# Optimization experiments

Measured on AMD Instinct MI355X. Metric: run time of the kernel, lower is better.

The kernel has to match this reference:

```python
import jax, jax.numpy as jnp
import numpy as np

B, S, D, H, E, K = 4, 1024, 1024, 4096, 8, 2

def setup_inputs() -> dict:
    key = jax.random.key(0)
    ks = jax.random.split(key, 6)
    sd = 1.0 / np.sqrt(D)
    sh = 1.0 / np.sqrt(H)
    return {
        "x": jax.random.normal(ks[0], (B, S, D), jnp.float32),
        "Wg": jax.random.normal(ks[1], (D, E), jnp.float32) * sd,
        "bg": jnp.zeros((E,), jnp.float32),
        "W1": jax.random.normal(ks[2], (E, D, H), jnp.float32) * sd,
        "b1": jnp.zeros((E, H), jnp.float32),
        "Wa": jax.random.normal(ks[3], (E, D, H), jnp.float32) * sd,
        "ba": jnp.zeros((E, H), jnp.float32),
        "W2": jax.random.normal(ks[4], (E, H, D), jnp.float32) * sh,
        "b2": jnp.zeros((E, D), jnp.float32),
        "kv_cache": 0,
    }

def reference(x, Wg, bg, W1, b1, Wa, ba, W2, b2, kv_cache):
    # gate: softmax over experts, top-k, renormalize
    gate = jax.nn.softmax(x @ Wg + bg, axis=-1)            # [B,S,E]
    w, idx = jax.lax.top_k(gate, K)                        # [B,S,K]
    w = w / jnp.sum(w, axis=-1, keepdims=True)
    # dense all-expert FF with SwiGLU: fc2( silu(fc_a(x)) * fc1(x) )
    a = jnp.einsum('bsd,edh->bseh', x, Wa) + ba            # [B,S,E,H]
    g = a * jax.nn.sigmoid(a)
    u = jnp.einsum('bsd,edh->bseh', x, W1) + b1
    y = jnp.einsum('bseh,ehd->bsed', g * u, W2) + b2       # [B,S,E,D]
    # gather top-k experts per token and combine
    sel = jnp.take_along_axis(y, idx[..., None], axis=2)   # [B,S,K,D]
    out = jnp.sum(sel * w[..., None], axis=-2)             # [B,S,D]
    return out
```

## Files before the change

### kernel.cpp

```cpp
#include <hip/hip_runtime.h>
#include <hip/hip_bf16.h>
#include <math.h>

#define TOKENS 4096
#define DD 1024
#define HH 4096
#define NE 8
#define PAIRS 8192
#define ROWCAP 8448
#define TCAP 72
#define G1_NT 32
#define G2_NT 128

typedef __bf16 bf16x8 __attribute__((ext_vector_type(8)));
typedef float f32x4 __attribute__((ext_vector_type(4)));

__device__ __forceinline__ unsigned short f2bf(float f) {
  union { float f; unsigned int u; } c; c.f = f;
  unsigned int x = c.u;
  return (unsigned short)((x + 0x7fffu + ((x >> 16) & 1u)) >> 16);
}

__device__ __forceinline__ void lds16(void* l, const void* g) {
  __builtin_amdgcn_global_load_lds((const __attribute__((address_space(1))) void*)g,
                                   (__attribute__((address_space(3))) void*)l, 16, 0, 0);
}

__global__ void init_kernel(int* counts) {
  if (threadIdx.x < NE) counts[threadIdx.x] = 0;
}

__global__ __launch_bounds__(256) void transpose_kernel(
    const float* __restrict__ Wa, const float* __restrict__ W1, const float* __restrict__ W2,
    unsigned short* __restrict__ WaT, unsigned short* __restrict__ W1T,
    unsigned short* __restrict__ W2T) {
  int b = blockIdx.x;
  int sec = b >> 13;
  int sb = b & 8191;
  const float* in; unsigned short* out; int R, C;
  if (sec == 0)      { in = Wa; out = WaT; R = DD; C = HH; }
  else if (sec == 1) { in = W1; out = W1T; R = DD; C = HH; }
  else               { in = W2; out = W2T; R = HH; C = DD; }
  int ntr = R >> 6, ntc = C >> 6;
  int per_e = ntr * ntc;
  int e = sb / per_e;
  int rem = sb - e * per_e;
  int tr = rem / ntc, tc = rem - (rem / ntc) * ntc;
  const float* ie = in + (size_t)e * R * C;
  unsigned short* oe = out + (size_t)e * R * C;

  __shared__ float t[64][68];
  int tid = threadIdx.x;
  int lr = tid >> 2;
  int c4 = (tid & 3) << 4;
  const float* src = ie + (size_t)(tr * 64 + lr) * C + tc * 64 + c4;
  float4 v0 = *(const float4*)(src);
  float4 v1 = *(const float4*)(src + 4);
  float4 v2 = *(const float4*)(src + 8);
  float4 v3 = *(const float4*)(src + 12);
  *(float4*)&t[lr][c4] = v0;
  *(float4*)&t[lr][c4 + 4] = v1;
  *(float4*)&t[lr][c4 + 8] = v2;
  *(float4*)&t[lr][c4 + 12] = v3;
  __syncthreads();

  int oc = tid >> 2;
  int r0 = (tid & 3) << 4;
  unsigned int pk[8];
#pragma unroll
  for (int i = 0; i < 8; i++) {
    unsigned int lo = f2bf(t[r0 + 2 * i][oc]);
    unsigned int hi = f2bf(t[r0 + 2 * i + 1][oc]);
    pk[i] = lo | (hi << 16);
  }
  unsigned short* dst = oe + (size_t)(tc * 64 + oc) * R + tr * 64 + r0;
  *(uint4*)(dst) = make_uint4(pk[0], pk[1], pk[2], pk[3]);
  *(uint4*)(dst + 8) = make_uint4(pk[4], pk[5], pk[6], pk[7]);
}

__global__ __launch_bounds__(256) void gate_kernel(const float* __restrict__ x,
    const float* __restrict__ Wg, const float* __restrict__ bg,
    int* __restrict__ counts, int* __restrict__ tok_e, int* __restrict__ tok_slot,
    float* __restrict__ tok_w) {
  int t = blockIdx.x, tid = threadIdx.x;
  const float* xr = x + (size_t)t * DD;
  float p[8] = {0, 0, 0, 0, 0, 0, 0, 0};
  for (int d = tid; d < DD; d += 256) {
    float xv = xr[d];
    const float4* wrow = (const float4*)(Wg + (size_t)d * NE);
    float4 w0 = wrow[0], w1 = wrow[1];
    p[0] += xv * w0.x; p[1] += xv * w0.y; p[2] += xv * w0.z; p[3] += xv * w0.w;
    p[4] += xv * w1.x; p[5] += xv * w1.y; p[6] += xv * w1.z; p[7] += xv * w1.w;
  }
#pragma unroll
  for (int e = 0; e < 8; e++) {
    p[e] += __shfl_down(p[e], 32);
    p[e] += __shfl_down(p[e], 16);
    p[e] += __shfl_down(p[e], 8);
    p[e] += __shfl_down(p[e], 4);
    p[e] += __shfl_down(p[e], 2);
    p[e] += __shfl_down(p[e], 1);
  }
  __shared__ float red[4][8];
  if ((tid & 63) == 0) {
#pragma unroll
    for (int e = 0; e < 8; e++) red[tid >> 6][e] = p[e];
  }
  __syncthreads();
  if (tid == 0) {
    float l[8];
#pragma unroll
    for (int e = 0; e < 8; e++) l[e] = red[0][e] + red[1][e] + red[2][e] + red[3][e] + bg[e];
    int e0 = 0; float l0 = l[0];
    for (int e = 1; e < 8; e++) if (l[e] > l0) { e0 = e; l0 = l[e]; }
    int e1 = -1; float l1 = -3.4e38f;
    for (int e = 0; e < 8; e++) if (e != e0 && l[e] > l1) { e1 = e; l1 = l[e]; }
    float w0 = 1.f / (1.f + __expf(l1 - l0));
    float w1 = 1.f - w0;
    int s0 = atomicAdd(&counts[e0], 1);
    int s1 = atomicAdd(&counts[e1], 1);
    tok_e[2 * t] = e0;     tok_slot[2 * t] = s0;     tok_w[2 * t] = w0;
    tok_e[2 * t + 1] = e1; tok_slot[2 * t + 1] = s1; tok_w[2 * t + 1] = w1;
  }
}

__global__ void scan_kernel(const int* __restrict__ counts, int* __restrict__ offsets,
                            int* __restrict__ tm_e, int* __restrict__ tm_row0,
                            int* __restrict__ tm_nrow, int* __restrict__ ntp) {
  if (threadIdx.x != 0 || blockIdx.x != 0) return;
  int c[NE];
#pragma unroll
  for (int e = 0; e < NE; e++) c[e] = counts[e];
  int off = 0, nt = 0;
  for (int e = 0; e < NE; e++) {
    offsets[e] = off;
    for (int r = 0; r < c[e]; r += 128) {
      tm_e[nt] = e; tm_row0[nt] = off + r;
      tm_nrow[nt] = (c[e] - r < 128) ? (c[e] - r) : 128;
      nt++;
    }
    off += c[e];
  }
  *ntp = nt;
}

__global__ __launch_bounds__(64) void gather_kernel(const float* __restrict__ x,
    const int* __restrict__ tok_e, const int* __restrict__ tok_slot,
    const float* __restrict__ tok_w, const int* __restrict__ offsets,
    unsigned short* __restrict__ Xe, int* __restrict__ pair_row, float* __restrict__ rw) {
  int pp = blockIdx.x, tid = threadIdx.x;
  int e = tok_e[pp];
  int row = offsets[e] + tok_slot[pp];
  int t = pp >> 1;
  const float* src = x + (size_t)t * DD + tid * 16;
  float4 v0 = *(const float4*)(src);
  float4 v1 = *(const float4*)(src + 4);
  float4 v2 = *(const float4*)(src + 8);
  float4 v3 = *(const float4*)(src + 12);
  unsigned int pk[8];
  pk[0] = f2bf(v0.x) | ((unsigned int)f2bf(v0.y) << 16);
  pk[1] = f2bf(v0.z) | ((unsigned int)f2bf(v0.w) << 16);
  pk[2] = f2bf(v1.x) | ((unsigned int)f2bf(v1.y) << 16);
  pk[3] = f2bf(v1.z) | ((unsigned int)f2bf(v1.w) << 16);
  pk[4] = f2bf(v2.x) | ((unsigned int)f2bf(v2.y) << 16);
  pk[5] = f2bf(v2.z) | ((unsigned int)f2bf(v2.w) << 16);
  pk[6] = f2bf(v3.x) | ((unsigned int)f2bf(v3.y) << 16);
  pk[7] = f2bf(v3.z) | ((unsigned int)f2bf(v3.w) << 16);
  unsigned short* dst = Xe + (size_t)row * DD + tid * 16;
  *(uint4*)(dst) = make_uint4(pk[0], pk[1], pk[2], pk[3]);
  *(uint4*)(dst + 8) = make_uint4(pk[4], pk[5], pk[6], pk[7]);
  if (tid == 0) { pair_row[pp] = row; rw[row] = tok_w[pp]; }
}


__global__ __launch_bounds__(256) void gemm1_kernel(
    const unsigned short* __restrict__ Xe,
    const unsigned short* __restrict__ WaT,
    const unsigned short* __restrict__ W1T,
    const float* __restrict__ ba, const float* __restrict__ b1,
    unsigned short* __restrict__ h,
    const int* __restrict__ tm_e, const int* __restrict__ tm_row0,
    const int* __restrict__ tm_nrow, const int* __restrict__ ntp) {
  __shared__ unsigned short sm[2][8192];

  int work = blockIdx.x;
  int tile = work >> 6;
  if (tile >= *ntp) return;
  int n0 = (work & 63) << 6;
  int e = tm_e[tile], row0 = tm_row0[tile], nrow = tm_nrow[tile];

  int tid = threadIdx.x;
  int lane = tid & 63, wid = tid >> 6;
  int wm = wid >> 1, wn = wid & 1;
  int fr = lane & 15, kc = lane >> 4;

  int srow = tid >> 2;
  int cd = tid & 3;
  int scl = (cd ^ ((srow >> 1) & 3)) << 3;

  const unsigned short* pA0 = Xe + (size_t)(row0 + srow) * DD + scl;
  const unsigned short* pA1 = Xe + (size_t)(row0 + 64 + srow) * DD + scl;
  const unsigned short* pBa = WaT + ((size_t)e << 22) + (size_t)(n0 + srow) * DD + scl;
  const unsigned short* pBu = W1T + ((size_t)e << 22) + (size_t)(n0 + srow) * DD + scl;

  unsigned short* ldst = &sm[0][0] + (size_t)tid * 8;

  int aof[4], bof[2];
#pragma unroll
  for (int m = 0; m < 4; m++) {
    int r = wm * 64 + m * 16 + fr;
    aof[m] = r * 64 + ((kc ^ ((r >> 1) & 3)) << 4);
  }
#pragma unroll
  for (int n = 0; n < 2; n++) {
    int r = wn * 32 + n * 16 + fr;
    bof[n] = 8192 + r * 64 + ((kc ^ ((r >> 1) & 3)) << 4);
  }

  f32x4 accA[4][2], accU[4][2];
  f32x4 z = {0.f, 0.f, 0.f, 0.f};
#pragma unroll
  for (int m = 0; m < 4; m++)
#pragma unroll
    for (int n = 0; n < 2; n++) { accA[m][n] = z; accU[m][n] = z; }

  auto stage = [&](int T, int buf) {
    int koff = (T < G1_NT ? T : G1_NT - 1) << 5;
    unsigned short* L = ldst + buf * 8192;
    lds16(L, pA0 + koff);
    lds16(L + 2048, pA1 + koff);
    lds16(L + 4096, pBa + koff);
    lds16(L + 6144, pBu + koff);
  };

  stage(0, 0);
  __syncthreads();
  int buf = 0;
  for (int T = 0; T < G1_NT; ++T) {
    stage(T + 1, buf ^ 1);
    const char* lb = (const char*)&sm[0][0] + (buf << 14);
    bf16x8 a[4], bA[2], bU[2];
#pragma unroll
    for (int m = 0; m < 4; m++) a[m] = *(const bf16x8*)(lb + aof[m]);
#pragma unroll
    for (int n = 0; n < 2; n++) {
      bA[n] = *(const bf16x8*)(lb + bof[n]);
      bU[n] = *(const bf16x8*)(lb + bof[n] + 4096);
    }
#pragma unroll
    for (int m = 0; m < 4; m++)
#pragma unroll
      for (int n = 0; n < 2; n++) {
        accA[m][n] = __builtin_amdgcn_mfma_f32_16x16x32_bf16(a[m], bA[n], accA[m][n], 0, 0, 0);
        accU[m][n] = __builtin_amdgcn_mfma_f32_16x16x32_bf16(a[m], bU[n], accU[m][n], 0, 0, 0);
      }
    __syncthreads();
    buf ^= 1;
  }

  int lr4 = kc * 4;
#pragma unroll
  for (int n = 0; n < 2; n++) {
    int col = n0 + wn * 32 + n * 16 + fr;
    float bav = ba[e * HH + col];
    float buv = b1[e * HH + col];
#pragma unroll
    for (int m = 0; m < 4; m++) {
#pragma unroll
      for (int j = 0; j < 4; j++) {
        int r = wm * 64 + m * 16 + lr4 + j;
        if (r < nrow) {
          float av = accA[m][n][j] + bav;
          float uv = accU[m][n][j] + buv;
          float s = __builtin_amdgcn_rcpf(1.f + __expf(-av));
          h[(size_t)(row0 + r) * HH + col] = f2bf(av * s * uv);
        }
      }
    }
  }
}

__global__ __launch_bounds__(256) void gemm2_kernel(
    const unsigned short* __restrict__ hb,
    const unsigned short* __restrict__ W2T,
    const float* __restrict__ b2, const float* __restrict__ rw,
    float* __restrict__ contrib,
    const int* __restrict__ tm_e, const int* __restrict__ tm_row0,
    const int* __restrict__ tm_nrow, const int* __restrict__ ntp) {
  __shared__ unsigned short sm[2][8192];

  int work = blockIdx.x;
  int tile = work >> 3;
  if (tile >= *ntp) return;
  int n0 = (work & 7) << 7;
  int e = tm_e[tile], row0 = tm_row0[tile], nrow = tm_nrow[tile];

  int tid = threadIdx.x;
  int lane = tid & 63, wid = tid >> 6;
  int wm = wid >> 1, wn = wid & 1;
  int fr = lane & 15, kc = lane >> 4;

  int srow = tid >> 2;
  int cd = tid & 3;
  int scl = (cd ^ ((srow >> 1) & 3)) << 3;

  const unsigned short* pA0 = hb + (size_t)(row0 + srow) * HH + scl;
  const unsigned short* pA1 = hb + (size_t)(row0 + 64 + srow) * HH + scl;
  const unsigned short* pB0 = W2T + ((size_t)e << 22) + (size_t)(n0 + srow) * HH + scl;
  const unsigned short* pB1 = W2T + ((size_t)e << 22) + (size_t)(n0 + 64 + srow) * HH + scl;

  unsigned short* ldst = &sm[0][0] + (size_t)tid * 8;

  int aof[4], bof[4];
#pragma unroll
  for (int m = 0; m < 4; m++) {
    int r = wm * 64 + m * 16 + fr;
    aof[m] = r * 64 + ((kc ^ ((r >> 1) & 3)) << 4);
  }
#pragma unroll
  for (int n = 0; n < 4; n++) {
    int r = wn * 64 + n * 16 + fr;
    bof[n] = 8192 + r * 64 + ((kc ^ ((r >> 1) & 3)) << 4);
  }

  f32x4 acc[4][4];
  f32x4 z = {0.f, 0.f, 0.f, 0.f};
#pragma unroll
  for (int m = 0; m < 4; m++)
#pragma unroll
    for (int n = 0; n < 4; n++) acc[m][n] = z;

  auto stage = [&](int T, int buf) {
    int koff = (T < G2_NT ? T : G2_NT - 1) << 5;
    unsigned short* L = ldst + buf * 8192;
    lds16(L, pA0 + koff);
    lds16(L + 2048, pA1 + koff);
    lds16(L + 4096, pB0 + koff);
    lds16(L + 6144, pB1 + koff);
  };

  stage(0, 0);
  __syncthreads();
  int buf = 0;
  for (int T = 0; T < G2_NT; ++T) {
    stage(T + 1, buf ^ 1);
    const char* lb = (const char*)&sm[0][0] + (buf << 14);
    bf16x8 a[4], b[4];
#pragma unroll
    for (int m = 0; m < 4; m++) a[m] = *(const bf16x8*)(lb + aof[m]);
#pragma unroll
    for (int n = 0; n < 4; n++) b[n] = *(const bf16x8*)(lb + bof[n]);
#pragma unroll
    for (int m = 0; m < 4; m++)
#pragma unroll
      for (int n = 0; n < 4; n++)
        acc[m][n] = __builtin_amdgcn_mfma_f32_16x16x32_bf16(a[m], b[n], acc[m][n], 0, 0, 0);
    __syncthreads();
    buf ^= 1;
  }

  float b2v[4];
#pragma unroll
  for (int n = 0; n < 4; n++) b2v[n] = b2[e * DD + n0 + wn * 64 + n * 16 + fr];
  int lr4 = kc * 4;
#pragma unroll
  for (int m = 0; m < 4; m++) {
#pragma unroll
    for (int j = 0; j < 4; j++) {
      int r = wm * 64 + m * 16 + lr4 + j;
      if (r < nrow) {
        float wv = rw[row0 + r];
        float* dst = contrib + (size_t)(row0 + r) * DD + n0 + wn * 64 + fr;
#pragma unroll
        for (int n = 0; n < 4; n++)
          dst[n * 16] = wv * (acc[m][n][j] + b2v[n]);
      }
    }
  }
}

__global__ __launch_bounds__(256) void combine_kernel(const float* __restrict__ contrib,
    const int* __restrict__ pair_row, float* __restrict__ out) {
  int t = blockIdx.x, tid = threadIdx.x;
  int r0 = pair_row[2 * t], r1 = pair_row[2 * t + 1];
  const float4* c0 = (const float4*)(contrib + (size_t)r0 * DD);
  const float4* c1 = (const float4*)(contrib + (size_t)r1 * DD);
  float4* o = (float4*)(out + (size_t)t * DD);
  float4 a = c0[tid], b = c1[tid];
  o[tid] = make_float4(a.x + b.x, a.y + b.y, a.z + b.z, a.w + b.w);
}

extern "C" void kernel_launch(void* const* d_in, const int* in_sizes, int n_in,
                              void* d_out, int out_size, void* d_ws, size_t ws_size,
                              hipStream_t stream) {
  const float* x  = (const float*)d_in[0];
  const float* Wg = (const float*)d_in[1];
  const float* bg = (const float*)d_in[2];
  const float* W1 = (const float*)d_in[3];
  const float* b1 = (const float*)d_in[4];
  const float* Wa = (const float*)d_in[5];
  const float* ba = (const float*)d_in[6];
  const float* W2 = (const float*)d_in[7];
  const float* b2 = (const float*)d_in[8];
  float* out = (float*)d_out;
  (void)in_sizes; (void)n_in; (void)out_size; (void)ws_size;

  char* p = (char*)d_ws;
  auto take = [&](size_t bytes) { char* r = p; p += (bytes + 255) & ~(size_t)255; return r; };
  unsigned short* WaT = (unsigned short*)take((size_t)NE * HH * DD * 2);
  unsigned short* W1T = (unsigned short*)take((size_t)NE * HH * DD * 2);
  unsigned short* W2T = (unsigned short*)take((size_t)NE * DD * HH * 2);
  unsigned short* Xe  = (unsigned short*)take((size_t)ROWCAP * DD * 2);
  unsigned short* hb  = (unsigned short*)take((size_t)ROWCAP * HH * 2);
  float* contrib      = (float*)take((size_t)ROWCAP * DD * 4);
  int* counts   = (int*)take(64);
  int* offsets  = (int*)take(64);
  int* tok_e    = (int*)take(PAIRS * 4);
  int* tok_slot = (int*)take(PAIRS * 4);
  float* tok_w  = (float*)take(PAIRS * 4);
  int* pair_row = (int*)take(PAIRS * 4);
  float* rw     = (float*)take(ROWCAP * 4);
  int* tm_e     = (int*)take(TCAP * 4);
  int* tm_row0  = (int*)take(TCAP * 4);
  int* tm_nrow  = (int*)take(TCAP * 4);
  int* ntp      = (int*)take(64);

  init_kernel<<<1, 64, 0, stream>>>(counts);
  transpose_kernel<<<3 * 8192, 256, 0, stream>>>(Wa, W1, W2, WaT, W1T, W2T);
  gate_kernel<<<TOKENS, 256, 0, stream>>>(x, Wg, bg, counts, tok_e, tok_slot, tok_w);
  scan_kernel<<<1, 64, 0, stream>>>(counts, offsets, tm_e, tm_row0, tm_nrow, ntp);
  gather_kernel<<<PAIRS, 64, 0, stream>>>(x, tok_e, tok_slot, tok_w, offsets, Xe, pair_row, rw);
  gemm1_kernel<<<TCAP * 64, 256, 0, stream>>>(Xe, WaT, W1T, ba, b1, hb, tm_e, tm_row0, tm_nrow, ntp);
  gemm2_kernel<<<TCAP * 8, 256, 0, stream>>>(hb, W2T, b2, rw, contrib, tm_e, tm_row0, tm_nrow, ntp);
  combine_kernel<<<TOKENS, 256, 0, stream>>>(contrib, pair_row, out);
}
```

Measured before the change: 556.8 us.

## Enlarge MoE GEMM tiles to 512-thread blocks with 256-row/256-col tiles

Both expert GEMMs move to 512-thread blocks with eight waves. GEMM1 now covers 256 token rows per tile, which needs a separate 256-row tile map from the scan kernel. GEMM2 now covers 256 output columns per tile. The aim is to reuse each staged weight and activation tile across more MFMA work, which cuts global/L2 traffic per FLOP. In exchange, LDS use per block grows to 48KB, there are fewer blocks to spread across CUs, and partially filled 256-row tiles waste more work.

```diff
diff --git a/kernel.cpp b/kernel.cpp
--- a/kernel.cpp
+++ b/kernel.cpp
@@ -8,6 +8,7 @@
 #define NE 8
 #define PAIRS 8192
 #define ROWCAP 8448
+#define T1CAP 40
 #define TCAP 72
 #define G1_NT 32
 #define G2_NT 128
@@ -125,23 +126,31 @@
 }
 
 __global__ void scan_kernel(const int* __restrict__ counts, int* __restrict__ offsets,
-                            int* __restrict__ tm_e, int* __restrict__ tm_row0,
-                            int* __restrict__ tm_nrow, int* __restrict__ ntp) {
+                            int* __restrict__ tm1_e, int* __restrict__ tm1_row0,
+                            int* __restrict__ tm1_nrow, int* __restrict__ ntp1,
+                            int* __restrict__ tm2_e, int* __restrict__ tm2_row0,
+                            int* __restrict__ tm2_nrow, int* __restrict__ ntp2) {
   if (threadIdx.x != 0 || blockIdx.x != 0) return;
   int c[NE];
 #pragma unroll
   for (int e = 0; e < NE; e++) c[e] = counts[e];
-  int off = 0, nt = 0;
+  int off = 0, n1 = 0, n2 = 0;
   for (int e = 0; e < NE; e++) {
     offsets[e] = off;
+    for (int r = 0; r < c[e]; r += 256) {
+      tm1_e[n1] = e; tm1_row0[n1] = off + r;
+      tm1_nrow[n1] = (c[e] - r < 256) ? (c[e] - r) : 256;
+      n1++;
+    }
     for (int r = 0; r < c[e]; r += 128) {
-      tm_e[nt] = e; tm_row0[nt] = off + r;
-      tm_nrow[nt] = (c[e] - r < 128) ? (c[e] - r) : 128;
-      nt++;
+      tm2_e[n2] = e; tm2_row0[n2] = off + r;
+      tm2_nrow[n2] = (c[e] - r < 128) ? (c[e] - r) : 128;
+      n2++;
     }
     off += c[e];
   }
-  *ntp = nt;
+  *ntp1 = n1;
+  *ntp2 = n2;
 }
 
 __global__ __launch_bounds__(64) void gather_kernel(const float* __restrict__ x,
@@ -173,7 +182,7 @@
 }
 
 
-__global__ __launch_bounds__(256) void gemm1_kernel(
+__global__ __launch_bounds__(512, 2) void gemm1_kernel(
     const unsigned short* __restrict__ Xe,
     const unsigned short* __restrict__ WaT,
     const unsigned short* __restrict__ W1T,
@@ -181,7 +190,7 @@
     unsigned short* __restrict__ h,
     const int* __restrict__ tm_e, const int* __restrict__ tm_row0,
     const int* __restrict__ tm_nrow, const int* __restrict__ ntp) {
-  __shared__ unsigned short sm[2][8192];
+  __shared__ unsigned short sm[2][12288];
 
   int work = blockIdx.x;
   int tile = work >> 6;
@@ -190,20 +199,24 @@
   int e = tm_e[tile], row0 = tm_row0[tile], nrow = tm_nrow[tile];
 
   int tid = threadIdx.x;
-  int lane = tid & 63, wid = tid >> 6;
-  int wm = wid >> 1, wn = wid & 1;
-  int fr = lane & 15, kc = lane >> 4;
-
-  int srow = tid >> 2;
-  int cd = tid & 3;
-  int scl = (cd ^ ((srow >> 1) & 3)) << 3;
-
-  const unsigned short* pA0 = Xe + (size_t)(row0 + srow) * DD + scl;
-  const unsigned short* pA1 = Xe + (size_t)(row0 + 64 + srow) * DD + scl;
-  const unsigned short* pBa = WaT + ((size_t)e << 22) + (size_t)(n0 + srow) * DD + scl;
-  const unsigned short* pBu = W1T + ((size_t)e << 22) + (size_t)(n0 + srow) * DD + scl;
-
-  unsigned short* ldst = &sm[0][0] + (size_t)tid * 8;
+  int l = tid & 63, w = tid >> 6;
+  int wm = w >> 1, wn = w & 1;
+  int fr = l & 15, kc = l >> 4;
+
+  int arow = (w << 4) + (l >> 2);
+  int cd = l & 3;
+  int swzA = (cd ^ ((arow >> 1) & 3)) << 3;
+  const unsigned short* pA1 = Xe + (size_t)(row0 + arow) * DD + swzA;
+  const unsigned short* pA2 = pA1 + (size_t)128 * DD;
+  int brow = (w < 4) ? arow : (arow - 64);
+  int swzB = (cd ^ ((brow >> 1) & 3)) << 3;
+  const unsigned short* pB = ((w < 4) ? WaT : W1T) + ((size_t)e << 22) +
+                             (size_t)(n0 + brow) * DD + swzB;
+
+  unsigned short* smb = &sm[0][0];
+  int dA1 = (w << 10) + (l << 4);
+  int dA2 = dA1 + 8192;
+  int dB  = 16384 + ((w & 3) << 10) + ((w >= 4) ? 4096 : 0) + (l << 4);
 
   int aof[4], bof[2];
 #pragma unroll
@@ -214,7 +227,7 @@
 #pragma unroll
   for (int n = 0; n < 2; n++) {
     int r = wn * 32 + n * 16 + fr;
-    bof[n] = 8192 + r * 64 + ((kc ^ ((r >> 1) & 3)) << 4);
+    bof[n] = 16384 + r * 64 + ((kc ^ ((r >> 1) & 3)) << 4);
   }
 
   f32x4 accA[4][2], accU[4][2];
@@ -226,11 +239,10 @@
 
   auto stage = [&](int T, int buf) {
     int koff = (T < G1_NT ? T : G1_NT - 1) << 5;
-    unsigned short* L = ldst + buf * 8192;
-    lds16(L, pA0 + koff);
-    lds16(L + 2048, pA1 + koff);
-    lds16(L + 4096, pBa + koff);
-    lds16(L + 6144, pBu + koff);
+    char* base = (char*)smb + buf * 24576;
+    lds16(base + dA1, pA1 + koff);
+    lds16(base + dA2, pA2 + koff);
+    lds16(base + dB,  pB  + koff);
   };
 
   stage(0, 0);
@@ -238,7 +250,7 @@
   int buf = 0;
   for (int T = 0; T < G1_NT; ++T) {
     stage(T + 1, buf ^ 1);
-    const char* lb = (const char*)&sm[0][0] + (buf << 14);
+    const char* lb = (const char*)smb + buf * 24576;
     bf16x8 a[4], bA[2], bU[2];
 #pragma unroll
     for (int m = 0; m < 4; m++) a[m] = *(const bf16x8*)(lb + aof[m]);
@@ -280,36 +292,37 @@
   }
 }
 
-__global__ __launch_bounds__(256) void gemm2_kernel(
+__global__ __launch_bounds__(512, 2) void gemm2_kernel(
     const unsigned short* __restrict__ hb,
     const unsigned short* __restrict__ W2T,
     const float* __restrict__ b2, const float* __restrict__ rw,
     float* __restrict__ contrib,
     const int* __restrict__ tm_e, const int* __restrict__ tm_row0,
     const int* __restrict__ tm_nrow, const int* __restrict__ ntp) {
-  __shared__ unsigned short sm[2][8192];
+  __shared__ unsigned short sm[2][12288];
 
   int work = blockIdx.x;
-  int tile = work >> 3;
+  int tile = work >> 2;
   if (tile >= *ntp) return;
-  int n0 = (work & 7) << 7;
+  int n0 = (work & 3) << 8;
   int e = tm_e[tile], row0 = tm_row0[tile], nrow = tm_nrow[tile];
 
   int tid = threadIdx.x;
-  int lane = tid & 63, wid = tid >> 6;
-  int wm = wid >> 1, wn = wid & 1;
-  int fr = lane & 15, kc = lane >> 4;
-
-  int srow = tid >> 2;
-  int cd = tid & 3;
-  int scl = (cd ^ ((srow >> 1) & 3)) << 3;
-
-  const unsigned short* pA0 = hb + (size_t)(row0 + srow) * HH + scl;
-  const unsigned short* pA1 = hb + (size_t)(row0 + 64 + srow) * HH + scl;
-  const unsigned short* pB0 = W2T + ((size_t)e << 22) + (size_t)(n0 + srow) * HH + scl;
-  const unsigned short* pB1 = W2T + ((size_t)e << 22) + (size_t)(n0 + 64 + srow) * HH + scl;
-
-  unsigned short* ldst = &sm[0][0] + (size_t)tid * 8;
+  int l = tid & 63, w = tid >> 6;
+  int wm = w >> 2, wn = w & 3;
+  int fr = l & 15, kc = l >> 4;
+
+  int arow = (w << 4) + (l >> 2);
+  int cd = l & 3;
+  int swzA = (cd ^ ((arow >> 1) & 3)) << 3;
+  const unsigned short* pA = hb + (size_t)(row0 + arow) * HH + swzA;
+  const unsigned short* pB1 = W2T + ((size_t)e << 22) + (size_t)(n0 + arow) * HH + swzA;
+  const unsigned short* pB2 = pB1 + (size_t)128 * HH;
+
+  unsigned short* smb = &sm[0][0];
+  int dA  = (w << 10) + (l << 4);
+  int dB1 = 8192 + (w << 10) + (l << 4);
+  int dB2 = dB1 + 8192;
 
   int aof[4], bof[4];
 #pragma unroll
@@ -319,8 +332,8 @@
   }
 #pragma unroll
   for (int n = 0; n < 4; n++) {
-    int r = wn * 64 + n * 16 + fr;
-    bof[n] = 8192 + r * 64 + ((kc ^ ((r >> 1) & 3)) << 4);
+    int rb = wn * 64 + n * 16 + fr;
+    bof[n] = 8192 + rb * 64 + ((kc ^ ((rb >> 1) & 3)) << 4);
   }
 
   f32x4 acc[4][4];
@@ -332,11 +345,10 @@
 
   auto stage = [&](int T, int buf) {
     int koff = (T < G2_NT ? T : G2_NT - 1) << 5;
-    unsigned short* L = ldst + buf * 8192;
-    lds16(L, pA0 + koff);
-    lds16(L + 2048, pA1 + koff);
-    lds16(L + 4096, pB0 + koff);
-    lds16(L + 6144, pB1 + koff);
+    char* base = (char*)smb + buf * 24576;
+    lds16(base + dA,  pA  + koff);
+    lds16(base + dB1, pB1 + koff);
+    lds16(base + dB2, pB2 + koff);
   };
 
   stage(0, 0);
@@ -344,7 +356,7 @@
   int buf = 0;
   for (int T = 0; T < G2_NT; ++T) {
     stage(T + 1, buf ^ 1);
-    const char* lb = (const char*)&sm[0][0] + (buf << 14);
+    const char* lb = (const char*)smb + buf * 24576;
     bf16x8 a[4], b[4];
 #pragma unroll
     for (int m = 0; m < 4; m++) a[m] = *(const bf16x8*)(lb + aof[m]);
@@ -420,17 +432,22 @@
   float* tok_w  = (float*)take(PAIRS * 4);
   int* pair_row = (int*)take(PAIRS * 4);
   float* rw     = (float*)take(ROWCAP * 4);
-  int* tm_e     = (int*)take(TCAP * 4);
-  int* tm_row0  = (int*)take(TCAP * 4);
-  int* tm_nrow  = (int*)take(TCAP * 4);
-  int* ntp      = (int*)take(64);
+  int* tm1_e    = (int*)take(T1CAP * 4);
+  int* tm1_row0 = (int*)take(T1CAP * 4);
+  int* tm1_nrow = (int*)take(T1CAP * 4);
+  int* ntp1     = (int*)take(64);
+  int* tm2_e    = (int*)take(TCAP * 4);
+  int* tm2_row0 = (int*)take(TCAP * 4);
+  int* tm2_nrow = (int*)take(TCAP * 4);
+  int* ntp2     = (int*)take(64);
 
   init_kernel<<<1, 64, 0, stream>>>(counts);
   transpose_kernel<<<3 * 8192, 256, 0, stream>>>(Wa, W1, W2, WaT, W1T, W2T);
   gate_kernel<<<TOKENS, 256, 0, stream>>>(x, Wg, bg, counts, tok_e, tok_slot, tok_w);
-  scan_kernel<<<1, 64, 0, stream>>>(counts, offsets, tm_e, tm_row0, tm_nrow, ntp);
+  scan_kernel<<<1, 64, 0, stream>>>(counts, offsets, tm1_e, tm1_row0, tm1_nrow, ntp1,
+                                    tm2_e, tm2_row0, tm2_nrow, ntp2);
   gather_kernel<<<PAIRS, 64, 0, stream>>>(x, tok_e, tok_slot, tok_w, offsets, Xe, pair_row, rw);
-  gemm1_kernel<<<TCAP * 64, 256, 0, stream>>>(Xe, WaT, W1T, ba, b1, hb, tm_e, tm_row0, tm_nrow, ntp);
-  gemm2_kernel<<<TCAP * 8, 256, 0, stream>>>(hb, W2T, b2, rw, contrib, tm_e, tm_row0, tm_nrow, ntp);
+  gemm1_kernel<<<T1CAP * 64, 512, 0, stream>>>(Xe, WaT, W1T, ba, b1, hb, tm1_e, tm1_row0, tm1_nrow, ntp1);
+  gemm2_kernel<<<TCAP * 4, 512, 0, stream>>>(hb, W2T, b2, rw, contrib, tm2_e, tm2_row0, tm2_nrow, ntp2);
   combine_kernel<<<TOKENS, 256, 0, stream>>>(contrib, pair_row, out);
 }
```

Result: slower. 574.1 us (+3.1%).
